# Performance work log

Measured on AMD Instinct MI355X. Metric: run time of the kernel, lower is better.

Reference implementation:

```python
import jax, jax.numpy as jnp
import numpy as np

WIDTH = 2048
NUM_HEADS = 16
HEAD_DIM = WIDTH // NUM_HEADS
WINDOW = 1024
B, T = 4, 2048
MIN_LOGIT = -2.3819763e+38
MAX_WAVELENGTH = 10000.0


def apply_rope(x, positions):
    # x: [b, t, n, h]; RoPE on first half of h, pass-through second half
    b, t, n, h = x.shape
    x_rope, x_pass = jnp.split(x, 2, axis=-1)
    half = x_rope.shape[-1] // 2
    freq_exponents = 2.0 * jnp.arange(half, dtype=jnp.float32) / (2 * half)
    inv_freq = MAX_WAVELENGTH ** (-freq_exponents)  # [half]
    sinusoid = positions.astype(jnp.float32).reshape(1, t, 1, 1) * inv_freq  # [1,t,1,half]
    sin = jnp.sin(sinusoid).astype(x.dtype)
    cos = jnp.cos(sinusoid).astype(x.dtype)
    x1, x2 = jnp.split(x_rope, 2, axis=-1)
    return jnp.concatenate([x1 * cos - x2 * sin, x2 * cos + x1 * sin, x_pass], axis=-1)


def setup_inputs() -> dict:
    key = jax.random.key(0)
    ks = jax.random.split(key, 6)
    x = jax.random.normal(ks[0], (B, T, WIDTH), dtype=jnp.float32)
    segment_pos = jnp.arange(T, dtype=jnp.int32)
    # forward-pass mask: single segment, causal + window
    pos = jnp.arange(T)
    attention_mask = (pos[:, None] >= pos[None, :]) & (pos[:, None] <= pos[None, :] + WINDOW)
    std = np.sqrt(1.0 / WIDTH)
    wq = jax.random.normal(ks[1], (WIDTH, WIDTH), dtype=jnp.float32) * std
    wk = jax.random.normal(ks[2], (HEAD_DIM, WIDTH), dtype=jnp.float32) * std
    wv = jax.random.normal(ks[3], (HEAD_DIM, WIDTH), dtype=jnp.float32) * std
    w_out = jax.random.normal(ks[4], (WIDTH, WIDTH), dtype=jnp.float32) * std
    b_out = jnp.zeros((WIDTH,), dtype=jnp.float32)
    return {"x": x, "segment_pos": segment_pos, "attention_mask": attention_mask,
            "wq": wq, "wk": wk, "wv": wv, "w_out": w_out, "b_out": b_out}


def reference(x, segment_pos, attention_mask, wq, wk, wv, w_out, b_out):
    b, t, _ = x.shape
    q = (x @ wq.T).reshape(b, t, NUM_HEADS, HEAD_DIM)  # [b,t,n,h]
    k = (x @ wk.T).reshape(b, t, 1, HEAD_DIM)          # single shared KV head (MQA)
    v = x @ wv.T                                        # [b,t,h]
    q = apply_rope(q, segment_pos)
    k = apply_rope(k, segment_pos)[:, :, 0]             # [b,t,h]
    logits = jnp.einsum('btnh,bsh->bnts', q, k).astype(jnp.float32) * (HEAD_DIM ** -0.5)
    logits = jnp.where(attention_mask[None, None], logits, MIN_LOGIT)
    probs = jax.nn.softmax(logits, axis=-1).astype(x.dtype)
    encoded = jnp.einsum('bnts,bsh->btnh', probs, v).reshape(b, t, WIDTH)
    return encoded @ w_out.T + b_out
```

## Files before the change

kernel.cpp:

```cpp
#include <hip/hip_runtime.h>
#include <stdint.h>


#define WIDTH_ 2048
#define NHEADS_ 16
#define HD_ 128
#define WINDOW_ 1024
#define B_ 4
#define T_ 2048
#define MROWS_ (B_ * T_)
#define NQKV_ (WIDTH_ + 2 * HD_)

typedef float f32x4 __attribute__((ext_vector_type(4)));
typedef __bf16 bf16x8 __attribute__((ext_vector_type(8)));
typedef float f32x4v __attribute__((ext_vector_type(4)));
typedef unsigned short u16;
typedef unsigned int u32;

__device__ __forceinline__ u16 f2bf(float x) {
  u32 u = __builtin_bit_cast(u32, x);
  return (u16)((u + 0x7FFFu + ((u >> 16) & 1u)) >> 16);
}
__device__ __forceinline__ float bf2f(u16 b) {
  u32 u = ((u32)b) << 16;
  return __builtin_bit_cast(float, u);
}
__device__ __forceinline__ u32 pack2bf(float a, float b) {
  union { __bf16 h[2]; u32 u; } c;
  c.h[0] = (__bf16)a; c.h[1] = (__bf16)b;
  return c.u;
}

__device__ __forceinline__ f32x4 mfma16(bf16x8 a, bf16x8 b, f32x4 c) {
  return __builtin_amdgcn_mfma_f32_16x16x32_bf16(a, b, c, 0, 0, 0);
}

#define GLL16(gp, lp)                                          \
  __builtin_amdgcn_global_load_lds(                            \
      (const __attribute__((address_space(1))) void*)(gp),     \
      (__attribute__((address_space(3))) void*)(lp), 16, 0, 0)

#define CSC_ 0.12753101296631838f
#define L2C_ 0.4152410118609203f

__global__ __launch_bounds__(256) void cvt_all(const float* __restrict__ x,
                                               const float* __restrict__ wq,
                                               const float* __restrict__ wk,
                                               const float* __restrict__ wv,
                                               const float* __restrict__ wo,
                                               u16* __restrict__ xb,
                                               u16* __restrict__ wqkv,
                                               u16* __restrict__ wob) {
  const int NX = MROWS_ * WIDTH_ / 4;
  const int NQ = WIDTH_ * WIDTH_ / 4;
  const int NK = HD_ * WIDTH_ / 4;
  const int total = NX + 2 * NQ + 2 * NK;
  int i = blockIdx.x * blockDim.x + threadIdx.x;
  int stride = gridDim.x * blockDim.x;
  for (; i < total; i += stride) {
    const float* s;
    u16* d;
    int j;
    if (i < NX) { s = x; d = xb; j = i; }
    else if (i < NX + NQ) { s = wq; d = wqkv; j = i - NX; }
    else if (i < NX + NQ + NK) { s = wk; d = wqkv + (size_t)WIDTH_ * WIDTH_; j = i - NX - NQ; }
    else if (i < NX + NQ + 2 * NK) { s = wv; d = wqkv + (size_t)(WIDTH_ + HD_) * WIDTH_; j = i - NX - NQ - NK; }
    else { s = wo; d = wob; j = i - NX - NQ - 2 * NK; }
    f32x4v v = *reinterpret_cast<const f32x4v*>(s + 4 * (size_t)j);
    uint2 o;
    o.x = (u32)f2bf(v[0]) | ((u32)f2bf(v[1]) << 16);
    o.y = (u32)f2bf(v[2]) | ((u32)f2bf(v[3]) << 16);
    *reinterpret_cast<uint2*>(d + 4 * (size_t)j) = o;
  }
}

__global__ __launch_bounds__(256) void gemm_bt64(const u16* __restrict__ A,
                                                 const u16* __restrict__ W,
                                                 u16* __restrict__ Cout,
                                                 int M, int N, int K) {
  __shared__ alignas(16) u16 As[128 * 32];
  __shared__ alignas(16) u16 Bs[64 * 32];
  const int tid = threadIdx.x;
  const int wid = tid >> 6, lane = tid & 63;
  const int g = lane >> 4, lr = lane & 15;
  const int m0 = blockIdx.y << 7, n0 = blockIdx.x << 6;
  const int wm = wid >> 1, wn = wid & 1;

  const f32x4 vzero = {0.f, 0.f, 0.f, 0.f};
  f32x4 acc[4][2];
#pragma unroll
  for (int i = 0; i < 4; i++)
#pragma unroll
    for (int j = 0; j < 2; j++) acc[i][j] = vzero;

  const int lrow = lane >> 2;
  const int lcol = (lane & 3) * 8;
  const u16* a0 = A + (size_t)(m0 + wid * 32 + lrow) * K + lcol;
  const u16* a1 = A + (size_t)(m0 + wid * 32 + 16 + lrow) * K + lcol;
  const u16* b0 = W + (size_t)(n0 + wid * 16 + lrow) * K + lcol;

  for (int k0 = 0; k0 < K; k0 += 32) {
    __syncthreads();
    GLL16(a0 + k0, &As[wid * 1024]);
    GLL16(a1 + k0, &As[wid * 1024 + 512]);
    GLL16(b0 + k0, &Bs[wid * 512]);
    __syncthreads();

    bf16x8 af[4], bfv[2];
#pragma unroll
    for (int mi = 0; mi < 4; mi++)
      af[mi] = *(const bf16x8*)&As[(wm * 64 + mi * 16 + lr) * 32 + g * 8];
#pragma unroll
    for (int ni = 0; ni < 2; ni++)
      bfv[ni] = *(const bf16x8*)&Bs[(wn * 32 + ni * 16 + lr) * 32 + g * 8];
#pragma unroll
    for (int mi = 0; mi < 4; mi++)
#pragma unroll
      for (int ni = 0; ni < 2; ni++)
        acc[mi][ni] = mfma16(af[mi], bfv[ni], acc[mi][ni]);
  }

#pragma unroll
  for (int mi = 0; mi < 4; mi++) {
    int row = m0 + wm * 64 + mi * 16 + g * 4;
#pragma unroll
    for (int ni = 0; ni < 2; ni++) {
      int col = n0 + wn * 32 + ni * 16 + lr;
#pragma unroll
      for (int r = 0; r < 4; r++)
        Cout[(size_t)(row + r) * N + col] = f2bf(acc[mi][ni][r]);
    }
  }
}

template <bool F32OUT>
__global__ __launch_bounds__(512, 2) void gemm256p8(const u16* __restrict__ A,
                                                    const u16* __restrict__ W,
                                                    void* __restrict__ Cout,
                                                    const float* __restrict__ bias,
                                                    int M, int N, int K) {
  __shared__ alignas(16) u16 As[2][2][128 * 64];
  __shared__ alignas(16) u16 Bs[2][2][128 * 64];
  const int tid = threadIdx.x;
  const int wid = tid >> 6, lane = tid & 63;
  const int g = lane >> 4, lr = lane & 15;
  const int wm = wid >> 2, wn = wid & 3;

  const int nwg = gridDim.x;
  const int o = blockIdx.x;
  const int wg = (o & 7) * (nwg >> 3) + (o >> 3);
  const int NT = N >> 8;
  const int mt = wg / NT, nt = wg % NT;
  const int m0 = mt << 8, n0 = nt << 8;

  const u16* pa[2];
  const u16* pb[2];
#pragma unroll
  for (int j = 0; j < 2; j++) {
    int ci = (wid + j * 8) * 64 + lane;
    int ri = ci >> 3, c = ci & 7;
    int colel = (c ^ (ri & 7)) * 8;
    int rA = ((ri >> 6) << 7) + (ri & 63);
    pa[j] = A + (size_t)(m0 + rA) * K + colel;
    pb[j] = W + (size_t)(n0 + ri) * K + colel;
  }
  const int dstoff = wid * 1024;

#define SA(bi, h, k0)                                                     \
  do {                                                                    \
    GLL16(pa[0] + (size_t)(h) * 64 * K + (k0), (char*)As[bi][h] + dstoff);\
    GLL16(pa[1] + (size_t)(h) * 64 * K + (k0),                            \
          (char*)As[bi][h] + dstoff + 8192);                              \
  } while (0)
#define SB(bi, h, k0)                                                     \
  do {                                                                    \
    GLL16(pb[0] + (size_t)(h) * 128 * K + (k0), (char*)Bs[bi][h] + dstoff);\
    GLL16(pb[1] + (size_t)(h) * 128 * K + (k0),                           \
          (char*)Bs[bi][h] + dstoff + 8192);                              \
  } while (0)

  const f32x4 vzero = {0.f, 0.f, 0.f, 0.f};
  f32x4 acc[8][4];
#pragma unroll
  for (int i = 0; i < 8; i++)
#pragma unroll
    for (int j = 0; j < 4; j++) acc[i][j] = vzero;

  bf16x8 bfv[4][2];

  auto LDA = [&](int bi, int mi, int kk) -> bf16x8 {
    int h = mi >> 2;
    int rb = wm * 64 + (mi & 3) * 16 + lr;
    return *(const bf16x8*)((const char*)As[bi][h] + rb * 128 +
                            (((kk * 4 + g) ^ (lr & 7)) << 4));
  };
  auto LDB = [&](int bi, int ni, int kk) -> bf16x8 {
    int rb = (wn & 1) * 64 + ni * 16 + lr;
    return *(const bf16x8*)((const char*)Bs[bi][wn >> 1] + rb * 128 +
                            (((kk * 4 + g) ^ (lr & 7)) << 4));
  };

#define VM6 asm volatile("s_waitcnt vmcnt(6)" ::: "memory")
#define VM0 asm volatile("s_waitcnt vmcnt(0)" ::: "memory")

#define PHASE(bi, p, STAGES, VM)                                          \
  {                                                                       \
    if ((p) == 0) {                                                       \
      for (int ni = 0; ni < 4; ni++)                                      \
        for (int kk = 0; kk < 2; kk++) bfv[ni][kk] = LDB(bi, ni, kk);     \
    }                                                                     \
    bf16x8 a0k0 = LDA(bi, 2 * (p), 0);                                    \
    bf16x8 a0k1 = LDA(bi, 2 * (p), 1);                                    \
    bf16x8 a1k0 = LDA(bi, 2 * (p) + 1, 0);                                \
    bf16x8 a1k1 = LDA(bi, 2 * (p) + 1, 1);                                \
    STAGES;                                                               \
    __builtin_amdgcn_s_barrier();                                         \
    asm volatile("s_waitcnt lgkmcnt(0)" ::: "memory");                    \
    __builtin_amdgcn_sched_barrier(0);                                    \
    __builtin_amdgcn_s_setprio(1);                                        \
    for (int ni = 0; ni < 4; ni++) {                                      \
      acc[2 * (p)][ni] = mfma16(a0k0, bfv[ni][0], acc[2 * (p)][ni]);      \
      acc[2 * (p)][ni] = mfma16(a0k1, bfv[ni][1], acc[2 * (p)][ni]);      \
      acc[2 * (p) + 1][ni] = mfma16(a1k0, bfv[ni][0], acc[2 * (p) + 1][ni]); \
      acc[2 * (p) + 1][ni] = mfma16(a1k1, bfv[ni][1], acc[2 * (p) + 1][ni]); \
    }                                                                     \
    __builtin_amdgcn_s_setprio(0);                                        \
    VM;                                                                   \
    __builtin_amdgcn_sched_barrier(0);                                    \
    __builtin_amdgcn_s_barrier();                                         \
  }

  SA(0, 0, 0); SA(0, 1, 0); SB(0, 0, 0); SB(0, 1, 0);
  SB(1, 0, 64); SB(1, 1, 64); SA(1, 0, 64);
  VM6;
  __builtin_amdgcn_sched_barrier(0);
  __builtin_amdgcn_s_barrier();

  const int half_iters = K >> 7;
  for (int i = 0; i < half_iters; ++i) {
    const bool pre = (i + 1 < half_iters);
    const int kc = i << 7;
    PHASE(0, 0, { SA(1, 1, kc + 64); }, );
    PHASE(0, 1, { if (pre) SB(0, 0, kc + 128); }, );
    PHASE(0, 2, { if (pre) SB(0, 1, kc + 128); }, );
    PHASE(0, 3, { if (pre) SA(0, 0, kc + 128); }, if (pre) { VM6; } else { VM0; });
    PHASE(1, 0, { if (pre) SA(0, 1, kc + 128); }, );
    PHASE(1, 1, { if (pre) SB(1, 0, kc + 192); }, );
    PHASE(1, 2, { if (pre) SB(1, 1, kc + 192); }, );
    PHASE(1, 3, { if (pre) SA(1, 0, kc + 192); }, if (pre) { VM6; } else { VM0; });
  }
#undef PHASE
#undef SA
#undef SB
#undef VM6
#undef VM0

#pragma unroll
  for (int mi = 0; mi < 8; mi++) {
    int row = m0 + wm * 128 + mi * 16 + g * 4;
#pragma unroll
    for (int ni = 0; ni < 4; ni++) {
      int col = n0 + wn * 64 + ni * 16 + lr;
#pragma unroll
      for (int r = 0; r < 4; r++) {
        float v = acc[mi][ni][r];
        if (F32OUT) {
          ((float*)Cout)[(size_t)(row + r) * N + col] = v + bias[col];
        } else {
          ((u16*)Cout)[(size_t)(row + r) * N + col] = f2bf(v);
        }
      }
    }
  }
}

__global__ __launch_bounds__(128) void kv_scatter(const u16* __restrict__ KVraw,
                                                  const int* __restrict__ segpos,
                                                  u16* __restrict__ Kb,
                                                  u16* __restrict__ VT,
                                                  float2* __restrict__ sc) {
  const int row = blockIdx.x;
  const int b = row / T_, t = row % T_;
  const float pos = (float)segpos[t];
  const u16* kvsrc = KVraw + (size_t)row * 256;
  const int tid = threadIdx.x;

  if (row < 512) {
    int idx = row * 128 + tid;
    int tt = idx >> 5, d = idx & 31;
    float ps = (float)segpos[tt];
    float ang = ps * exp2f(-(float)d * L2C_);
    float2 v;
    v.x = cosf(ang);
    v.y = sinf(ang);
    sc[idx] = v;
  }

  if (tid < 32) {
    int d = tid;
    float inv = exp2f(-(float)d * L2C_);
    float ang = pos * inv;
    float sn = sinf(ang), cs = cosf(ang);
    float x1 = bf2f(kvsrc[d]), x2 = bf2f(kvsrc[d + 32]);
    Kb[(size_t)row * HD_ + d] = f2bf(x1 * cs - x2 * sn);
    Kb[(size_t)row * HD_ + d + 32] = f2bf(x2 * cs + x1 * sn);
  } else if (tid >= 64 && tid < 128) {
    int d = tid;
    Kb[(size_t)row * HD_ + d] = kvsrc[d];
  }
  for (int j = tid; j < HD_; j += 128) {
    VT[((size_t)b * HD_ + j) * T_ + t] = kvsrc[HD_ + j];
  }
}

__global__ __launch_bounds__(512, 4) void attn(const u16* __restrict__ Qraw,
                                               const float2* __restrict__ sc,
                                               const u16* __restrict__ Kb,
                                               const u16* __restrict__ VT,
                                               u16* __restrict__ Eb) {
  __shared__ alignas(16) u16 Ks[2][64 * 128];
  __shared__ alignas(16) u16 Vs[2][128 * 64];
  __shared__ alignas(16) u16 Ps[8][16 * 64];

  const int tid = threadIdx.x;
  const int wid = tid >> 6, lane = tid & 63;
  const int g = lane >> 4, lr = lane & 15;

  const int bid = blockIdx.x;
  const int grp = bid >> 4;
  const int b = grp >> 4, n = grp & 15;
  const int qt = ((bid & 15) + b * 4) & 15;
  const int q0b = qt * 128;
  const int q0w = q0b + wid * 16;
  const int q = q0w + lr;

  const char* kptr = (const char*)(Kb + (size_t)b * T_ * HD_);
  const char* vptr = (const char*)(VT + (size_t)b * HD_ * T_);

  const char* srcb[4];
  int smul, dst0;
  if (wid < 4) {
    smul = HD_ * 2;
#pragma unroll
    for (int i = 0; i < 4; i++) {
      int row = wid * 16 + i * 4 + (lane >> 4);
      int c = (lane & 15) << 4;
      srcb[i] = kptr + (size_t)row * 256 + (c ^ ((row & 7) << 4));
    }
    dst0 = wid * 4096;
  } else {
    smul = 2;
#pragma unroll
    for (int i = 0; i < 4; i++) {
      int row = (wid - 4) * 32 + i * 8 + (lane >> 3);
      int c = (lane & 7) << 4;
      srcb[i] = vptr + (size_t)row * (T_ * 2) + (c ^ ((row & 7) << 4));
    }
    dst0 = (wid - 4) * 4096;
  }

  bf16x8 qf[4];
  {
    const float2* scp = sc + (size_t)q * 32 + g * 8;
    const u16* qp = Qraw + (size_t)(b * T_ + q) * WIDTH_ + n * HD_;
    bf16x8 r0 = *(const bf16x8*)(qp + g * 8);
    bf16x8 r1 = *(const bf16x8*)(qp + 32 + g * 8);
    bf16x8 r2 = *(const bf16x8*)(qp + 64 + g * 8);
    bf16x8 r3 = *(const bf16x8*)(qp + 96 + g * 8);
#pragma unroll
    for (int j = 0; j < 8; j++) {
      float2 cs2 = scp[j];
      float x1 = (float)r0[j], x2 = (float)r1[j];
      qf[0][j] = (__bf16)((x1 * cs2.x - x2 * cs2.y) * CSC_);
      qf[1][j] = (__bf16)((x2 * cs2.x + x1 * cs2.y) * CSC_);
      qf[2][j] = (__bf16)((float)r2[j] * CSC_);
      qf[3][j] = (__bf16)((float)r3[j] * CSC_);
    }
  }

  const f32x4 vzero = {0.f, 0.f, 0.f, 0.f};
  f32x4 eacc[8];
#pragma unroll
  for (int i = 0; i < 8; i++) eacc[i] = vzero;
  float m_r = -1e30f, l_r = 0.f;

  const int sbeg = (q0b > WINDOW_) ? (q0b - WINDOW_) : 0;
  const int nt = (q0b + 127 - sbeg) / 64 + 1;

  char* Pw = (char*)Ps[wid];
  const int swz = (lr & 7) << 4;

  auto STAGE = [&](int s0, int buf) {
    char* dbase = (wid < 4) ? ((char*)Ks[buf] + dst0) : ((char*)Vs[buf] + dst0);
#pragma unroll
    for (int i = 0; i < 4; i++) {
      GLL16(srcb[i] + (size_t)s0 * smul, dbase + i * 1024);
    }
  };

  STAGE(sbeg, 0);
  __syncthreads();

  for (int t = 0; t < nt; ++t) {
    const int s0 = sbeg + t * 64;
    const int cur = t & 1;
    if (t + 1 < nt) STAGE(s0 + 64, cur ^ 1);

    const bool active = (s0 <= q0w + 15) && (s0 + 63 >= q0w - WINDOW_);
    if (active) {
      const char* kB = (const char*)Ks[cur];
      const char* vB = (const char*)Vs[cur];
      f32x4 sacc[4];
#pragma unroll
      for (int h = 0; h < 4; h++) sacc[h] = vzero;
#pragma unroll
      for (int h = 0; h < 4; h++) {
        const int krow = h * 16 + lr;
#pragma unroll
        for (int kk = 0; kk < 4; kk++) {
          bf16x8 kf = *(const bf16x8*)(kB + krow * 256 + ((kk * 64 + g * 16) ^ swz));
          sacc[h] = mfma16(kf, qf[kk], sacc[h]);
        }
      }

      const bool wint = (s0 + 63 <= q0w) && (s0 >= q0w + 15 - WINDOW_);
      float pm = -1e30f;
      if (wint) {
#pragma unroll
        for (int h = 0; h < 4; h++)
#pragma unroll
          for (int r = 0; r < 4; r++) pm = fmaxf(pm, sacc[h][r]);
      } else {
#pragma unroll
        for (int h = 0; h < 4; h++)
#pragma unroll
          for (int r = 0; r < 4; r++) {
            int s = s0 + h * 16 + g * 4 + r;
            bool ok = (s <= q) && (s + WINDOW_ >= q);
            float v = ok ? sacc[h][r] : -1e30f;
            sacc[h][r] = v;
            pm = fmaxf(pm, v);
          }
      }
      pm = fmaxf(pm, __shfl_xor(pm, 16));
      pm = fmaxf(pm, __shfl_xor(pm, 32));

      if (!__all(pm <= m_r + 8.f)) {
        float mnew = fmaxf(m_r, pm);
        float alpha = exp2f(m_r - mnew);
        m_r = mnew;
        l_r *= alpha;
        float aq[4];
#pragma unroll
        for (int r = 0; r < 4; r++) aq[r] = __shfl(alpha, g * 4 + r);
#pragma unroll
        for (int i = 0; i < 8; i++) {
          f32x4 e = eacc[i];
#pragma unroll
          for (int r = 0; r < 4; r++) e[r] *= aq[r];
          eacc[i] = e;
        }
      }
      float rs = 0.f;
#pragma unroll
      for (int h = 0; h < 4; h++)
#pragma unroll
        for (int r = 0; r < 4; r++) {
          float e = exp2f(sacc[h][r] - m_r);
          sacc[h][r] = e;
          rs += e;
        }
      rs += __shfl_xor(rs, 16);
      rs += __shfl_xor(rs, 32);
      l_r += rs;

#pragma unroll
      for (int h = 0; h < 4; h++) {
        int base = (lr * 128 + h * 32 + g * 8) ^ swz;
        uint2 w2;
        w2.x = pack2bf(sacc[h][0], sacc[h][1]);
        w2.y = pack2bf(sacc[h][2], sacc[h][3]);
        *(uint2*)(Pw + base) = w2;
      }
      bf16x8 pf0 = *(const bf16x8*)(Pw + ((lr * 128 + g * 16) ^ swz));
      bf16x8 pf1 = *(const bf16x8*)(Pw + ((lr * 128 + 64 + g * 16) ^ swz));

#pragma unroll
      for (int ht = 0; ht < 8; ht++) {
        const int vrow = ht * 16 + lr;
        bf16x8 vf0 = *(const bf16x8*)(vB + vrow * 128 + ((g * 16) ^ swz));
        bf16x8 vf1 = *(const bf16x8*)(vB + vrow * 128 + ((64 + g * 16) ^ swz));
        eacc[ht] = mfma16(pf0, vf0, eacc[ht]);
        eacc[ht] = mfma16(pf1, vf1, eacc[ht]);
      }
    }
    __syncthreads();
  }

  float lq[4];
#pragma unroll
  for (int r = 0; r < 4; r++) lq[r] = 1.f / __shfl(l_r, g * 4 + r);
#pragma unroll
  for (int ht = 0; ht < 8; ht++) {
#pragma unroll
    for (int r = 0; r < 4; r++) {
      int row = b * T_ + q0w + g * 4 + r;
      int col = n * HD_ + ht * 16 + lr;
      Eb[(size_t)row * WIDTH_ + col] = f2bf(eacc[ht][r] * lq[r]);
    }
  }
}

extern "C" void kernel_launch(void* const* d_in, const int* in_sizes, int n_in,
                              void* d_out, int out_size, void* d_ws, size_t ws_size,
                              hipStream_t stream) {
  (void)in_sizes; (void)n_in; (void)out_size; (void)ws_size;
  const float* x = (const float*)d_in[0];
  const int* segpos = (const int*)d_in[1];
  const float* wq = (const float*)d_in[3];
  const float* wk = (const float*)d_in[4];
  const float* wv = (const float*)d_in[5];
  const float* w_out = (const float*)d_in[6];
  const float* b_out = (const float*)d_in[7];

  char* p = (char*)d_ws;
  u16* xb = (u16*)p;    p += (size_t)MROWS_ * WIDTH_ * 2;
  u16* wqkv = (u16*)p;  p += (size_t)NQKV_ * WIDTH_ * 2;
  u16* wob = (u16*)p;   p += (size_t)WIDTH_ * WIDTH_ * 2;
  u16* qraw = (u16*)p;  p += (size_t)MROWS_ * WIDTH_ * 2;
  u16* kvraw = (u16*)p; p += (size_t)MROWS_ * 256 * 2;
  u16* kb = (u16*)p;    p += (size_t)MROWS_ * HD_ * 2;
  u16* vt = (u16*)p;    p += (size_t)B_ * HD_ * T_ * 2;
  float2* sc = (float2*)p; p += (size_t)T_ * 32 * 8;
  u16* eb = xb;

  cvt_all<<<4096, 256, 0, stream>>>(x, wq, wk, wv, w_out, xb, wqkv, wob);

  gemm256p8<false><<<(MROWS_ / 256) * (WIDTH_ / 256), 512, 0, stream>>>(
      xb, wqkv, qraw, nullptr, MROWS_, WIDTH_, WIDTH_);
  gemm_bt64<<<dim3(256 / 64, MROWS_ / 128), 256, 0, stream>>>(
      xb, wqkv + (size_t)WIDTH_ * WIDTH_, kvraw, MROWS_, 256, WIDTH_);

  kv_scatter<<<MROWS_, 128, 0, stream>>>(kvraw, segpos, kb, vt, sc);
  attn<<<B_ * NHEADS_ * (T_ / 128), 512, 0, stream>>>(qraw, sc, kb, vt, eb);

  gemm256p8<true><<<(MROWS_ / 256) * (WIDTH_ / 256), 512, 0, stream>>>(
      eb, wob, d_out, b_out, MROWS_, WIDTH_, WIDTH_);
}
```

Measured before the change: 309.0 us.

## Give each attention wave two 16-row query subtiles with 32-wide KV tiles

The attention kernel now runs 4 waves of 256 threads instead of 8, and each wave handles 32 query rows as two 16-row subtiles. Every K and V fragment read from LDS is reused across both subtiles, and the KV tile shrinks to 32 keys so LDS use per block drops. The cost is roughly twice the accumulator registers per wave and twice as many loop iterations with barriers. The V staging also drops its XOR swizzle, which may cause LDS bank conflicts.

```diff
diff --git a/kernel.cpp b/kernel.cpp
--- a/kernel.cpp
+++ b/kernel.cpp
@@ -313,14 +313,14 @@
   }
 }
 
-__global__ __launch_bounds__(512, 4) void attn(const u16* __restrict__ Qraw,
+__global__ __launch_bounds__(256, 4) void attn(const u16* __restrict__ Qraw,
                                                const float2* __restrict__ sc,
                                                const u16* __restrict__ Kb,
                                                const u16* __restrict__ VT,
                                                u16* __restrict__ Eb) {
-  __shared__ alignas(16) u16 Ks[2][64 * 128];
-  __shared__ alignas(16) u16 Vs[2][128 * 64];
-  __shared__ alignas(16) u16 Ps[8][16 * 64];
+  __shared__ alignas(16) u16 Ks[2][32 * 128];
+  __shared__ alignas(16) u16 Vs[2][128 * 32];
+  __shared__ alignas(16) u16 Ps[4][2][16 * 32];
 
   const int tid = threadIdx.x;
   const int wid = tid >> 6, lane = tid & 63;
@@ -331,20 +331,20 @@
   const int b = grp >> 4, n = grp & 15;
   const int qt = ((bid & 15) + b * 4) & 15;
   const int q0b = qt * 128;
-  const int q0w = q0b + wid * 16;
-  const int q = q0w + lr;
+  const int q0w = q0b + wid * 32;
 
   const char* kptr = (const char*)(Kb + (size_t)b * T_ * HD_);
   const char* vptr = (const char*)(VT + (size_t)b * HD_ * T_);
 
   const char* srcb[4];
   int smul, dst0;
-  if (wid < 4) {
+  if (wid < 2) {
     smul = HD_ * 2;
 #pragma unroll
     for (int i = 0; i < 4; i++) {
-      int row = wid * 16 + i * 4 + (lane >> 4);
-      int c = (lane & 15) << 4;
+      int ci = wid * 256 + i * 64 + lane;
+      int row = ci >> 4;
+      int c = (ci & 15) << 4;
       srcb[i] = kptr + (size_t)row * 256 + (c ^ ((row & 7) << 4));
     }
     dst0 = wid * 4096;
@@ -352,17 +352,20 @@
     smul = 2;
 #pragma unroll
     for (int i = 0; i < 4; i++) {
-      int row = (wid - 4) * 32 + i * 8 + (lane >> 3);
-      int c = (lane & 7) << 4;
-      srcb[i] = vptr + (size_t)row * (T_ * 2) + (c ^ ((row & 7) << 4));
-    }
-    dst0 = (wid - 4) * 4096;
-  }
-
-  bf16x8 qf[4];
-  {
-    const float2* scp = sc + (size_t)q * 32 + g * 8;
-    const u16* qp = Qraw + (size_t)(b * T_ + q) * WIDTH_ + n * HD_;
+      int ci = (wid - 2) * 256 + i * 64 + lane;
+      int row = ci >> 2;
+      int colb = (ci & 3) << 4;
+      srcb[i] = vptr + (size_t)row * (T_ * 2) + colb;
+    }
+    dst0 = (wid - 2) * 4096;
+  }
+
+  bf16x8 qf[2][4];
+#pragma unroll
+  for (int su = 0; su < 2; su++) {
+    const int qq = q0w + su * 16 + lr;
+    const float2* scp = sc + (size_t)qq * 32 + g * 8;
+    const u16* qp = Qraw + (size_t)(b * T_ + qq) * WIDTH_ + n * HD_;
     bf16x8 r0 = *(const bf16x8*)(qp + g * 8);
     bf16x8 r1 = *(const bf16x8*)(qp + 32 + g * 8);
     bf16x8 r2 = *(const bf16x8*)(qp + 64 + g * 8);
@@ -371,27 +374,28 @@
     for (int j = 0; j < 8; j++) {
       float2 cs2 = scp[j];
       float x1 = (float)r0[j], x2 = (float)r1[j];
-      qf[0][j] = (__bf16)((x1 * cs2.x - x2 * cs2.y) * CSC_);
-      qf[1][j] = (__bf16)((x2 * cs2.x + x1 * cs2.y) * CSC_);
-      qf[2][j] = (__bf16)((float)r2[j] * CSC_);
-      qf[3][j] = (__bf16)((float)r3[j] * CSC_);
+      qf[su][0][j] = (__bf16)((x1 * cs2.x - x2 * cs2.y) * CSC_);
+      qf[su][1][j] = (__bf16)((x2 * cs2.x + x1 * cs2.y) * CSC_);
+      qf[su][2][j] = (__bf16)((float)r2[j] * CSC_);
+      qf[su][3][j] = (__bf16)((float)r3[j] * CSC_);
     }
   }
 
   const f32x4 vzero = {0.f, 0.f, 0.f, 0.f};
-  f32x4 eacc[8];
-#pragma unroll
-  for (int i = 0; i < 8; i++) eacc[i] = vzero;
-  float m_r = -1e30f, l_r = 0.f;
+  f32x4 eacc[2][8];
+#pragma unroll
+  for (int su = 0; su < 2; su++)
+#pragma unroll
+    for (int i = 0; i < 8; i++) eacc[su][i] = vzero;
+  float m_r[2] = {-1e30f, -1e30f}, l_r[2] = {0.f, 0.f};
 
   const int sbeg = (q0b > WINDOW_) ? (q0b - WINDOW_) : 0;
-  const int nt = (q0b + 127 - sbeg) / 64 + 1;
+  const int ntt = (q0b + 127 - sbeg) / 32 + 1;
 
   char* Pw = (char*)Ps[wid];
-  const int swz = (lr & 7) << 4;
 
   auto STAGE = [&](int s0, int buf) {
-    char* dbase = (wid < 4) ? ((char*)Ks[buf] + dst0) : ((char*)Vs[buf] + dst0);
+    char* dbase = (wid < 2) ? ((char*)Ks[buf] + dst0) : ((char*)Vs[buf] + dst0);
 #pragma unroll
     for (int i = 0; i < 4; i++) {
       GLL16(srcb[i] + (size_t)s0 * smul, dbase + i * 1024);
@@ -401,112 +405,127 @@
   STAGE(sbeg, 0);
   __syncthreads();
 
-  for (int t = 0; t < nt; ++t) {
-    const int s0 = sbeg + t * 64;
+  for (int t = 0; t < ntt; ++t) {
+    const int s0 = sbeg + t * 32;
     const int cur = t & 1;
-    if (t + 1 < nt) STAGE(s0 + 64, cur ^ 1);
-
-    const bool active = (s0 <= q0w + 15) && (s0 + 63 >= q0w - WINDOW_);
+    if (t + 1 < ntt) STAGE(s0 + 32, cur ^ 1);
+
+    const bool active = (s0 <= q0w + 31) && (s0 + 31 >= q0w - WINDOW_);
     if (active) {
       const char* kB = (const char*)Ks[cur];
       const char* vB = (const char*)Vs[cur];
-      f32x4 sacc[4];
-#pragma unroll
-      for (int h = 0; h < 4; h++) sacc[h] = vzero;
-#pragma unroll
-      for (int h = 0; h < 4; h++) {
+
+      f32x4 sacc[2][2];
+#pragma unroll
+      for (int su = 0; su < 2; su++)
+#pragma unroll
+        for (int h = 0; h < 2; h++) sacc[su][h] = vzero;
+#pragma unroll
+      for (int h = 0; h < 2; h++) {
+        bf16x8 kf[4];
         const int krow = h * 16 + lr;
-#pragma unroll
-        for (int kk = 0; kk < 4; kk++) {
-          bf16x8 kf = *(const bf16x8*)(kB + krow * 256 + ((kk * 64 + g * 16) ^ swz));
-          sacc[h] = mfma16(kf, qf[kk], sacc[h]);
+        const int swz = (lr & 7) << 4;
+#pragma unroll
+        for (int kk = 0; kk < 4; kk++)
+          kf[kk] = *(const bf16x8*)(kB + krow * 256 + ((kk * 64 + g * 16) ^ swz));
+#pragma unroll
+        for (int su = 0; su < 2; su++)
+#pragma unroll
+          for (int kk = 0; kk < 4; kk++)
+            sacc[su][h] = mfma16(kf[kk], qf[su][kk], sacc[su][h]);
+      }
+
+      const bool wint = (s0 + 31 <= q0w) && (s0 >= q0w + 31 - WINDOW_);
+#pragma unroll
+      for (int su = 0; su < 2; su++) {
+        const int qq = q0w + su * 16 + lr;
+        float pm = -1e30f;
+        if (wint) {
+#pragma unroll
+          for (int h = 0; h < 2; h++)
+#pragma unroll
+            for (int r = 0; r < 4; r++) pm = fmaxf(pm, sacc[su][h][r]);
+        } else {
+#pragma unroll
+          for (int h = 0; h < 2; h++)
+#pragma unroll
+            for (int r = 0; r < 4; r++) {
+              int s = s0 + h * 16 + g * 4 + r;
+              bool ok = (s <= qq) && (s + WINDOW_ >= qq);
+              float v = ok ? sacc[su][h][r] : -1e30f;
+              sacc[su][h][r] = v;
+              pm = fmaxf(pm, v);
+            }
+        }
+        pm = fmaxf(pm, __shfl_xor(pm, 16));
+        pm = fmaxf(pm, __shfl_xor(pm, 32));
+        if (!__all(pm <= m_r[su] + 8.f)) {
+          float mnew = fmaxf(m_r[su], pm);
+          float alpha = exp2f(m_r[su] - mnew);
+          m_r[su] = mnew;
+          l_r[su] *= alpha;
+          float aq[4];
+#pragma unroll
+          for (int r = 0; r < 4; r++) aq[r] = __shfl(alpha, g * 4 + r);
+#pragma unroll
+          for (int i = 0; i < 8; i++) {
+            f32x4 e = eacc[su][i];
+#pragma unroll
+            for (int r = 0; r < 4; r++) e[r] *= aq[r];
+            eacc[su][i] = e;
+          }
+        }
+        float rs = 0.f;
+#pragma unroll
+        for (int h = 0; h < 2; h++)
+#pragma unroll
+          for (int r = 0; r < 4; r++) {
+            float e = exp2f(sacc[su][h][r] - m_r[su]);
+            sacc[su][h][r] = e;
+            rs += e;
+          }
+        rs += __shfl_xor(rs, 16);
+        rs += __shfl_xor(rs, 32);
+        l_r[su] += rs;
+
+#pragma unroll
+        for (int h = 0; h < 2; h++) {
+          uint2 w2;
+          w2.x = pack2bf(sacc[su][h][0], sacc[su][h][1]);
+          w2.y = pack2bf(sacc[su][h][2], sacc[su][h][3]);
+          *(uint2*)(Pw + su * 1024 + lr * 64 + h * 32 + g * 8) = w2;
         }
       }
 
-      const bool wint = (s0 + 63 <= q0w) && (s0 >= q0w + 15 - WINDOW_);
-      float pm = -1e30f;
-      if (wint) {
-#pragma unroll
-        for (int h = 0; h < 4; h++)
-#pragma unroll
-          for (int r = 0; r < 4; r++) pm = fmaxf(pm, sacc[h][r]);
-      } else {
-#pragma unroll
-        for (int h = 0; h < 4; h++)
-#pragma unroll
-          for (int r = 0; r < 4; r++) {
-            int s = s0 + h * 16 + g * 4 + r;
-            bool ok = (s <= q) && (s + WINDOW_ >= q);
-            float v = ok ? sacc[h][r] : -1e30f;
-            sacc[h][r] = v;
-            pm = fmaxf(pm, v);
-          }
-      }
-      pm = fmaxf(pm, __shfl_xor(pm, 16));
-      pm = fmaxf(pm, __shfl_xor(pm, 32));
-
-      if (!__all(pm <= m_r + 8.f)) {
-        float mnew = fmaxf(m_r, pm);
-        float alpha = exp2f(m_r - mnew);
-        m_r = mnew;
-        l_r *= alpha;
-        float aq[4];
-#pragma unroll
-        for (int r = 0; r < 4; r++) aq[r] = __shfl(alpha, g * 4 + r);
-#pragma unroll
-        for (int i = 0; i < 8; i++) {
-          f32x4 e = eacc[i];
-#pragma unroll
-          for (int r = 0; r < 4; r++) e[r] *= aq[r];
-          eacc[i] = e;
-        }
-      }
-      float rs = 0.f;
-#pragma unroll
-      for (int h = 0; h < 4; h++)
-#pragma unroll
-        for (int r = 0; r < 4; r++) {
-          float e = exp2f(sacc[h][r] - m_r);
-          sacc[h][r] = e;
-          rs += e;
-        }
-      rs += __shfl_xor(rs, 16);
-      rs += __shfl_xor(rs, 32);
-      l_r += rs;
-
-#pragma unroll
-      for (int h = 0; h < 4; h++) {
-        int base = (lr * 128 + h * 32 + g * 8) ^ swz;
-        uint2 w2;
-        w2.x = pack2bf(sacc[h][0], sacc[h][1]);
-        w2.y = pack2bf(sacc[h][2], sacc[h][3]);
-        *(uint2*)(Pw + base) = w2;
-      }
-      bf16x8 pf0 = *(const bf16x8*)(Pw + ((lr * 128 + g * 16) ^ swz));
-      bf16x8 pf1 = *(const bf16x8*)(Pw + ((lr * 128 + 64 + g * 16) ^ swz));
-
+      bf16x8 pf[2];
+#pragma unroll
+      for (int su = 0; su < 2; su++)
+        pf[su] = *(const bf16x8*)(Pw + su * 1024 + lr * 64 + g * 16);
 #pragma unroll
       for (int ht = 0; ht < 8; ht++) {
         const int vrow = ht * 16 + lr;
-        bf16x8 vf0 = *(const bf16x8*)(vB + vrow * 128 + ((g * 16) ^ swz));
-        bf16x8 vf1 = *(const bf16x8*)(vB + vrow * 128 + ((64 + g * 16) ^ swz));
-        eacc[ht] = mfma16(pf0, vf0, eacc[ht]);
-        eacc[ht] = mfma16(pf1, vf1, eacc[ht]);
+        bf16x8 vf = *(const bf16x8*)(vB + vrow * 64 + g * 16);
+#pragma unroll
+        for (int su = 0; su < 2; su++)
+          eacc[su][ht] = mfma16(pf[su], vf, eacc[su][ht]);
       }
     }
     __syncthreads();
   }
 
-  float lq[4];
-#pragma unroll
-  for (int r = 0; r < 4; r++) lq[r] = 1.f / __shfl(l_r, g * 4 + r);
-#pragma unroll
-  for (int ht = 0; ht < 8; ht++) {
-#pragma unroll
-    for (int r = 0; r < 4; r++) {
-      int row = b * T_ + q0w + g * 4 + r;
-      int col = n * HD_ + ht * 16 + lr;
-      Eb[(size_t)row * WIDTH_ + col] = f2bf(eacc[ht][r] * lq[r]);
+#pragma unroll
+  for (int su = 0; su < 2; su++) {
+    float lq[4];
+#pragma unroll
+    for (int r = 0; r < 4; r++) lq[r] = 1.f / __shfl(l_r[su], g * 4 + r);
+#pragma unroll
+    for (int ht = 0; ht < 8; ht++) {
+#pragma unroll
+      for (int r = 0; r < 4; r++) {
+        int row = b * T_ + q0w + su * 16 + g * 4 + r;
+        int col = n * HD_ + ht * 16 + lr;
+        Eb[(size_t)row * WIDTH_ + col] = f2bf(eacc[su][ht][r] * lq[r]);
+      }
     }
   }
 }
@@ -542,7 +561,7 @@
       xb, wqkv + (size_t)WIDTH_ * WIDTH_, kvraw, MROWS_, 256, WIDTH_);
 
   kv_scatter<<<MROWS_, 128, 0, stream>>>(kvraw, segpos, kb, vt, sc);
-  attn<<<B_ * NHEADS_ * (T_ / 128), 512, 0, stream>>>(qraw, sc, kb, vt, eb);
+  attn<<<B_ * NHEADS_ * (T_ / 128), 256, 0, stream>>>(qraw, sc, kb, vt, eb);
 
   gemm256p8<true><<<(MROWS_ / 256) * (WIDTH_ / 256), 512, 0, stream>>>(
       eb, wob, d_out, b_out, MROWS_, WIDTH_, WIDTH_);
```

New measurement: 585.6 us. 89.5% more time.
